# Performance work log

Hardware: AMD Instinct MI355X
Metric: run time of the kernel (lower is better)

## Reference

```python
import jax, jax.numpy as jnp
import numpy as np

B, I, H, O, K = 256, 512, 512, 512, 256


def setup_inputs() -> dict:
    key = jax.random.key(0)
    ks = jax.random.split(key, 16)
    def lin(kw, kb, out_dim, in_dim):
        s = 1.0 / np.sqrt(in_dim)
        W = jax.random.uniform(kw, (out_dim, in_dim), jnp.float32, -s, s)
        b = jax.random.uniform(kb, (out_dim,), jnp.float32, -s, s)
        return W, b
    Wd, bd = lin(ks[0], ks[1], H, I + 2 * H)
    Wr, br = lin(ks[2], ks[3], H, I + H)
    Wz, bz = lin(ks[4], ks[5], H, I + H)
    Wh, bh = lin(ks[6], ks[7], H, I + H)
    Wo, bo = lin(ks[8], ks[9], O, H)
    return {
        "sample": jax.random.normal(ks[10], (B, I), jnp.float32),
        "hidden": jax.random.normal(ks[11], (B, H), jnp.float32),
        "hidden_tensor": jax.random.normal(ks[12], (K, B, H), jnp.float32),
        "d_0": jax.random.normal(ks[13], (B, H), jnp.float32),
        "Wd": Wd, "bd": bd, "Wr": Wr, "br": br,
        "Wz": Wz, "bz": bz, "Wh": Wh, "bh": bh, "Wo": Wo, "bo": bo,
    }


def _filter_d(hidden_tensor, d_values):
    # get_ws: w[j] = prod_{m=0}^{K-1-j} (m - d) / (m + 1)  for j in [0, K)
    # Vectorized: cumprod of (m-d)/(m+1) along m, then flip.
    m = jnp.arange(K, dtype=d_values.dtype).reshape(K, 1, 1)  # [K,1,1]
    factors = (m - d_values[None, :, :]) / (m + 1.0)          # [K,B,H]
    w = jnp.flip(jnp.cumprod(factors, axis=0), axis=0)        # [K,B,H]
    return jnp.sum(hidden_tensor * w, axis=0)                 # [B,H]


def reference(sample, hidden, hidden_tensor, d_0,
              Wd, bd, Wr, br, Wz, bz, Wh, bh, Wo, bo):
    combined = jnp.concatenate([sample, hidden], axis=1)          # [B, I+H]
    combined_d = jnp.concatenate([sample, hidden, d_0], axis=1)   # [B, I+2H]

    d_values = jax.nn.sigmoid(combined_d @ Wd.T + bd) * 0.5       # [B,H]
    first = -_filter_d(hidden_tensor, d_values)                   # [B,H]

    r_gate = jax.nn.sigmoid(combined @ Wr.T + br)
    z_gate = jax.nn.sigmoid(combined @ Wz.T + bz)

    combined2 = jnp.concatenate([sample, r_gate * hidden], axis=1)
    h_tilde = jnp.tanh(combined2 @ Wh.T + bh)
    second = h_tilde * (1.0 - z_gate)

    hidden_new = first + second                                   # [B,H]
    h_c_1 = jnp.concatenate([hidden_tensor, hidden_new[None]], axis=0)[1:]  # [K,B,H]
    output = hidden_new @ Wo.T + bo                               # [B,O]
    return (output, hidden_new, h_c_1, d_values)
```

## Files before the change

### kernel.cpp

```cpp
#include <hip/hip_runtime.h>
#include <cstddef>

#define B_ 256
#define H_ 512
#define KF 256
#define BH 131072
#define BH2 65536
#define BH4 32768
#define H4 128

#define BM 64
#define BN 64
#define BK 16

__device__ __forceinline__ float sigmoidf_(float x) { return 1.0f / (1.0f + __expf(-x)); }
__device__ __forceinline__ float tanh_fast(float x) { return 2.0f / (1.0f + __expf(-2.0f * x)) - 1.0f; }
__device__ __forceinline__ float4 sig4(float4 v) {
    return make_float4(sigmoidf_(v.x), sigmoidf_(v.y), sigmoidf_(v.z), sigmoidf_(v.w));
}

#define MAC_LOOP()                                                         \
    _Pragma("unroll")                                                      \
    for (int kk = 0; kk < BK; ++kk) {                                      \
        const float4 a = *(const float4*)&As[kk][ty << 2];                 \
        const float4 w = *(const float4*)&Ws[kk][tx << 2];                 \
        const float a4[4] = {a.x, a.y, a.z, a.w};                          \
        const float w4[4] = {w.x, w.y, w.z, w.w};                          \
        _Pragma("unroll")                                                  \
        for (int i = 0; i < 4; ++i)                                        \
            _Pragma("unroll")                                              \
            for (int j = 0; j < 4; ++j)                                    \
                acc[i][j] = fmaf(a4[i], w4[j], acc[i][j]);                 \
    }

template<bool MUL>
__device__ __forceinline__ void gemm64(
    float (*As)[BM + 4], float (*Ws)[BN + 4],
    const float* __restrict__ abase, const float* __restrict__ rbase,
    const float* __restrict__ W, int Ktot, int ks,
    int bm, int bn, int nIter, float* __restrict__ p)
{
    const int tid = threadIdx.x;
    const int ty = tid >> 4, tx = tid & 15;
    const int lrow = tid >> 2, lcol = (tid & 3) << 2;
    const float* aptr = abase + (bm + lrow) * 512 + lcol;
    const float* rptr = MUL ? rbase + (bm + lrow) * 512 + lcol : nullptr;
    const float* wptr = W + (size_t)(bn + lrow) * Ktot + ks + lcol;

    float acc[4][4] = {};
    float4 av = *(const float4*)aptr;
    if (MUL) { const float4 rv = *(const float4*)rptr;
               av.x *= rv.x; av.y *= rv.y; av.z *= rv.z; av.w *= rv.w; }
    float4 wv = *(const float4*)wptr;

    for (int it = 0; it < nIter; ++it) {
        __syncthreads();
        As[lcol + 0][lrow] = av.x; As[lcol + 1][lrow] = av.y;
        As[lcol + 2][lrow] = av.z; As[lcol + 3][lrow] = av.w;
        Ws[lcol + 0][lrow] = wv.x; Ws[lcol + 1][lrow] = wv.y;
        Ws[lcol + 2][lrow] = wv.z; Ws[lcol + 3][lrow] = wv.w;
        __syncthreads();
        if (it < nIter - 1) {
            av = *(const float4*)(aptr + (it + 1) * BK);
            if (MUL) { const float4 rv = *(const float4*)(rptr + (it + 1) * BK);
                       av.x *= rv.x; av.y *= rv.y; av.z *= rv.z; av.w *= rv.w; }
            wv = *(const float4*)(wptr + (it + 1) * BK);
        }
        MAC_LOOP();
    }
    #pragma unroll
    for (int i = 0; i < 4; ++i) {
        const int m = bm + (ty << 2) + i;
        #pragma unroll
        for (int j = 0; j < 4; ++j)
            p[m * 512 + bn + (tx << 2) + j] = acc[i][j];
    }
}

__global__ __launch_bounds__(256) void k_gemm_drz(
    const float* __restrict__ sample, const float* __restrict__ hidden,
    const float* __restrict__ d0,
    const float* __restrict__ Wd, const float* __restrict__ Wr,
    const float* __restrict__ Wz,
    float* __restrict__ dbase, float* __restrict__ rzbase)
{
    __shared__ float As[BK][BM + 4];
    __shared__ float Ws[BK][BN + 4];
    const int z = blockIdx.z;
    if (z < 6) {
        const int ks = z << 8, seg = ks >> 9;
        const float* ab = (seg == 0 ? sample : (seg == 1 ? hidden : d0)) + (ks & 511);
        gemm64<false>(As, Ws, ab, nullptr, Wd, 1536, ks,
                      blockIdx.y * BM, blockIdx.x * BN, 16, dbase + (size_t)z * BH);
    } else {
        const int id = z - 6, gz = id >> 2, s = id & 3, ks = s << 8;
        const float* ab = (ks < 512 ? sample + ks : hidden + (ks - 512));
        gemm64<false>(As, Ws, ab, nullptr, gz ? Wz : Wr, 1024, ks,
                      blockIdx.y * BM, blockIdx.x * BN, 16, rzbase + (size_t)id * BH);
    }
}

__global__ __launch_bounds__(256) void k_dv(
    const float4* __restrict__ dparts, const float4* __restrict__ bd,
    const float4* __restrict__ rzparts, const float4* __restrict__ br,
    const float4* __restrict__ bz,
    float4* __restrict__ dv4, float4* __restrict__ rb4, float4* __restrict__ zb4)
{
    const int g = blockIdx.x * 256 + threadIdx.x;
    const int n = g & (H4 - 1);
    float4 sd = bd[n], sr = br[n], sz = bz[n];
    #pragma unroll
    for (int s = 0; s < 6; ++s) { const float4 p = dparts[(size_t)s * BH4 + g];
        sd.x += p.x; sd.y += p.y; sd.z += p.z; sd.w += p.w; }
    #pragma unroll
    for (int s = 0; s < 4; ++s) { const float4 p = rzparts[(size_t)s * BH4 + g];
        sr.x += p.x; sr.y += p.y; sr.z += p.z; sr.w += p.w; }
    #pragma unroll
    for (int s = 4; s < 8; ++s) { const float4 p = rzparts[(size_t)s * BH4 + g];
        sz.x += p.x; sz.y += p.y; sz.z += p.z; sz.w += p.w; }
    const float4 d = sig4(sd);
    dv4[g] = make_float4(0.5f * d.x, 0.5f * d.y, 0.5f * d.z, 0.5f * d.w);
    rb4[g] = sig4(sr);
    zb4[g] = sig4(sz);
}

__global__ __launch_bounds__(256) void k_gemm_h(
    const float* __restrict__ sample, const float* __restrict__ hidden,
    const float* __restrict__ rb, const float* __restrict__ Wh,
    float* __restrict__ parts)
{
    __shared__ float As[BK][BM + 4];
    __shared__ float Ws[BK][BN + 4];
    const int s = blockIdx.z, ks = s << 8;
    if (ks < 512)
        gemm64<false>(As, Ws, sample + ks, nullptr, Wh, 1024, ks,
                      blockIdx.y * BM, blockIdx.x * BN, 16, parts + (size_t)s * BH);
    else
        gemm64<true>(As, Ws, hidden + (ks - 512), rb + (ks - 512), Wh, 1024, ks,
                     blockIdx.y * BM, blockIdx.x * BN, 16, parts + (size_t)s * BH);
}

#define FLOADB(buf, b)                                                     \
    _Pragma("unroll")                                                      \
    for (int u = 0; u < 8; ++u)                                            \
        buf[u] = ld_base[-(ptrdiff_t)((b) * 8 + u) * BH4];

#define FCSTORE(buf, b)                                                    \
    _Pragma("unroll")                                                      \
    for (int u = 0; u < 8; ++u) {                                          \
        const int t = t0 + (b) * 8 + u;                                    \
        const float iv = s_inv[t], tv = s_tinv[t];                         \
        c.x *= fmaf(-d.x, iv, tv); c.y *= fmaf(-d.y, iv, tv);              \
        c.z *= fmaf(-d.z, iv, tv); c.w *= fmaf(-d.w, iv, tv);              \
        a.x = fmaf(buf[u].x, c.x, a.x); a.y = fmaf(buf[u].y, c.y, a.y);    \
        a.z = fmaf(buf[u].z, c.z, a.z); a.w = fmaf(buf[u].w, c.w, a.w);    \
        st_base[-(ptrdiff_t)((b) * 8 + u) * BH4] = buf[u];                 \
    }

__global__ __launch_bounds__(256) void k_filter(
    const float4* __restrict__ ht4, const float4* __restrict__ dv4,
    float4* __restrict__ acc_out, float4* __restrict__ hc14)
{
    __shared__ float s_inv[KF], s_tinv[KF];
    const int tid = threadIdx.x;
    const float fi = 1.0f / (float)(tid + 1);
    s_inv[tid] = fi; s_tinv[tid] = (float)tid * fi;
    __syncthreads();

    const int seg = blockIdx.x >> 7;
    const int q   = ((blockIdx.x & 127) << 8) | tid;
    const float4 d = dv4[q];
    const int t0 = seg << 6;

    const float4* ld_base = ht4 + (size_t)(255 - t0) * BH4 + q;
    float4*       st_base = hc14 + (ptrdiff_t)(254 - t0) * BH4 + q;

    float4 c = make_float4(1.f, 1.f, 1.f, 1.f);
    float4 a = make_float4(0.f, 0.f, 0.f, 0.f);

    float4 va[8], vb[8];
    FLOADB(va, 0);
    #pragma unroll
    for (int b = 0; b < 8; b += 2) {
        FLOADB(vb, b + 1);
        FCSTORE(va, b);
        if (b + 2 < 8) { FLOADB(va, b + 2); }
        FCSTORE(vb, b + 1);
    }
    acc_out[(size_t)seg * BH4 + q] = a;
}

__global__ __launch_bounds__(256) void k_finalize(
    const float4* __restrict__ dv4, const float4* __restrict__ ws4,
    const float4* __restrict__ bh, const float4* __restrict__ zb4,
    float4* hc1_4, float4* __restrict__ hn_out)
{
    __shared__ float s_inv[192], s_tinv[192];
    const int tid = threadIdx.x;
    if (tid < 192) { const float fi = 1.0f / (float)(tid + 1);
                     s_inv[tid] = fi; s_tinv[tid] = (float)tid * fi; }
    __syncthreads();

    const int g = blockIdx.x * 256 + tid;
    const int n = g & (H4 - 1);
    const float4 d = dv4[g];

    float4 c = make_float4(1.f, 1.f, 1.f, 1.f), px0, px1, px2;
    #pragma unroll 16
    for (int t = 0; t < 64; ++t) {
        const float iv = s_inv[t], tv = s_tinv[t];
        c.x *= fmaf(-d.x, iv, tv); c.y *= fmaf(-d.y, iv, tv);
        c.z *= fmaf(-d.z, iv, tv); c.w *= fmaf(-d.w, iv, tv);
    }
    px0 = c;
    #pragma unroll 16
    for (int t = 64; t < 128; ++t) {
        const float iv = s_inv[t], tv = s_tinv[t];
        c.x *= fmaf(-d.x, iv, tv); c.y *= fmaf(-d.y, iv, tv);
        c.z *= fmaf(-d.z, iv, tv); c.w *= fmaf(-d.w, iv, tv);
    }
    px1 = c;
    #pragma unroll 16
    for (int t = 128; t < 192; ++t) {
        const float iv = s_inv[t], tv = s_tinv[t];
        c.x *= fmaf(-d.x, iv, tv); c.y *= fmaf(-d.y, iv, tv);
        c.z *= fmaf(-d.z, iv, tv); c.w *= fmaf(-d.w, iv, tv);
    }
    px2 = c;

    const float4 a0 = ws4[(size_t)4 * BH4 + g];
    const float4 a1 = ws4[(size_t)5 * BH4 + g];
    const float4 a2 = ws4[(size_t)6 * BH4 + g];
    const float4 a3 = ws4[(size_t)7 * BH4 + g];
    float4 hs = bh[n];
    #pragma unroll
    for (int s = 0; s < 4; ++s) { const float4 p = ws4[(size_t)s * BH4 + g];
        hs.x += p.x; hs.y += p.y; hs.z += p.z; hs.w += p.w; }
    const float4 z = zb4[g];

    float4 hn;
    hn.x = tanh_fast(hs.x) * (1.0f - z.x)
         - (a0.x + px0.x * a1.x + px1.x * a2.x + px2.x * a3.x);
    hn.y = tanh_fast(hs.y) * (1.0f - z.y)
         - (a0.y + px0.y * a1.y + px1.y * a2.y + px2.y * a3.y);
    hn.z = tanh_fast(hs.z) * (1.0f - z.z)
         - (a0.z + px0.z * a1.z + px1.z * a2.z + px2.z * a3.z);
    hn.w = tanh_fast(hs.w) * (1.0f - z.w)
         - (a0.w + px0.w * a1.w + px1.w * a2.w + px2.w * a3.w);
    hn_out[g] = hn;
    hc1_4[(size_t)255 * BH4 + g] = hn;
}

__global__ __launch_bounds__(256) void k_gemm_o(
    const float* __restrict__ hn, const float* __restrict__ Wo,
    float* __restrict__ parts, int chunk)
{
    __shared__ float As[BK][BM + 4];
    __shared__ float Ws[BK][BN + 4];
    const int s = blockIdx.z, ks = s * chunk;
    gemm64<false>(As, Ws, hn + ks, nullptr, Wo, 512, ks,
                  blockIdx.y * BM, blockIdx.x * BN, chunk / BK, parts + (size_t)s * BH);
}

__global__ __launch_bounds__(256) void k_reduce_o(
    const float4* parts, const float4* __restrict__ bo, float4* out, int NS)
{
    const int g = blockIdx.x * 256 + threadIdx.x;
    float4 v = bo[g & (H4 - 1)];
    for (int s = 0; s < NS; ++s) { const float4 p = parts[(size_t)s * BH4 + g];
        v.x += p.x; v.y += p.y; v.z += p.z; v.w += p.w; }
    out[g] = v;
}

__global__ __launch_bounds__(256) void k_reduce_rz(
    const float4* __restrict__ parts, const float4* __restrict__ br,
    const float4* __restrict__ bz, float4* __restrict__ rb, float4* __restrict__ zb)
{
    const int g = blockIdx.x * 256 + threadIdx.x;
    const int n = g & (H4 - 1);
    float4 r = br[n], z = bz[n];
    #pragma unroll
    for (int s = 0; s < 4; ++s) { const float4 p = parts[(size_t)s * BH4 + g];
        r.x += p.x; r.y += p.y; r.z += p.z; r.w += p.w; }
    #pragma unroll
    for (int s = 4; s < 8; ++s) { const float4 p = parts[(size_t)s * BH4 + g];
        z.x += p.x; z.y += p.y; z.z += p.z; z.w += p.w; }
    rb[g] = sig4(r); zb[g] = sig4(z);
}

__global__ __launch_bounds__(256) void k_filter_full(
    const float* __restrict__ ht, const float* dparts, const float* __restrict__ bd,
    const float* zbuf, const float* hparts, const float* __restrict__ bh,
    float* hc1, float* __restrict__ dv_out, float* __restrict__ hn_out)
{
    __shared__ float s_inv[KF], s_tinv[KF];
    const int tid = threadIdx.x;
    const float fi = 1.0f / (float)(tid + 1);
    s_inv[tid] = fi; s_tinv[tid] = (float)tid * fi;
    __syncthreads();

    const int g = blockIdx.x * 256 + tid;
    const int n = g & (H_ - 1);
    float sd = bd[n];
    #pragma unroll
    for (int s = 0; s < 6; ++s) sd += dparts[(size_t)s * BH + g];
    const float d = 0.5f * sigmoidf_(sd);
    dv_out[g] = d;
    float sh = bh[n];
    #pragma unroll
    for (int s = 0; s < 4; ++s) sh += hparts[(size_t)s * BH + g];
    const float z = zbuf[g];

    float c = 1.0f, acc = 0.0f;
    #pragma unroll 16
    for (int t = 0; t < KF; ++t) {
        const int k = KF - 1 - t;
        const float v = ht[(size_t)k * BH + g];
        c *= fmaf(-d, s_inv[t], s_tinv[t]);
        acc = fmaf(v, c, acc);
        if (k >= 1) hc1[(size_t)(k - 1) * BH + g] = v;
    }
    const float hn = tanh_fast(sh) * (1.0f - z) - acc;
    hc1[(size_t)(KF - 1) * BH + g] = hn;
    hn_out[g] = hn;
}

extern "C" void kernel_launch(void* const* d_in, const int* in_sizes, int n_in,
                              void* d_out, int out_size, void* d_ws, size_t ws_size,
                              hipStream_t stream)
{
    const float* sample = (const float*)d_in[0];
    const float* hidden = (const float*)d_in[1];
    const float* ht     = (const float*)d_in[2];
    const float* d0     = (const float*)d_in[3];
    const float* Wd = (const float*)d_in[4];
    const float* bd = (const float*)d_in[5];
    const float* Wr = (const float*)d_in[6];
    const float* br = (const float*)d_in[7];
    const float* Wz = (const float*)d_in[8];
    const float* bz = (const float*)d_in[9];
    const float* Wh = (const float*)d_in[10];
    const float* bh = (const float*)d_in[11];
    const float* Wo = (const float*)d_in[12];
    const float* bo = (const float*)d_in[13];

    float* out     = (float*)d_out;
    float* out_o   = out;
    float* out_hn  = out + BH;
    float* out_hc1 = out + 2 * BH;
    float* out_dv  = out + 2 * BH + (size_t)KF * BH;

    const size_t slice = BH;
    const size_t need = 10ull * slice * sizeof(float);

    if (ws_size >= need) {
        float* ws = (float*)d_ws;
        float* rb = ws + 8 * slice;
        float* zb = ws + 9 * slice;

        k_gemm_drz<<<dim3(8, 4, 14), 256, 0, stream>>>(sample, hidden, d0,
                                                       Wd, Wr, Wz, out_hc1, ws);
        k_dv<<<dim3(128), 256, 0, stream>>>(
            (const float4*)out_hc1, (const float4*)bd,
            (const float4*)ws, (const float4*)br, (const float4*)bz,
            (float4*)out_dv, (float4*)rb, (float4*)zb);
        k_gemm_h<<<dim3(8, 4, 4), 256, 0, stream>>>(sample, hidden, rb, Wh, ws);
        k_filter<<<dim3(512), 256, 0, stream>>>(
            (const float4*)ht, (const float4*)out_dv,
            (float4*)(ws + 4 * slice), (float4*)out_hc1);
        k_finalize<<<dim3(128), 256, 0, stream>>>(
            (const float4*)out_dv, (const float4*)ws,
            (const float4*)bh, (const float4*)zb,
            (float4*)out_hc1, (float4*)out_hn);
        k_gemm_o<<<dim3(8, 4, 4), 256, 0, stream>>>(out_hn, Wo, ws, 128);
        k_reduce_o<<<dim3(128), 256, 0, stream>>>((const float4*)ws,
                                                  (const float4*)bo,
                                                  (float4*)out_o, 4);
    } else {
        float* sl = out_hc1;
        k_gemm_drz<<<dim3(8, 4, 14), 256, 0, stream>>>(sample, hidden, d0,
                                                       Wd, Wr, Wz, sl, sl + 6 * slice);
        k_reduce_rz<<<dim3(128), 256, 0, stream>>>((const float4*)(sl + 6 * slice),
                                                   (const float4*)br, (const float4*)bz,
                                                   (float4*)(sl + 14 * slice),
                                                   (float4*)(sl + 15 * slice));
        k_gemm_h<<<dim3(8, 4, 4), 256, 0, stream>>>(sample, hidden, sl + 14 * slice, Wh,
                                                    sl + 16 * slice);
        k_filter_full<<<dim3(512), 256, 0, stream>>>(ht, sl, bd, sl + 15 * slice,
                                                     sl + 16 * slice, bh,
                                                     out_hc1, out_dv, out_hn);
        k_gemm_o<<<dim3(8, 4, 1), 256, 0, stream>>>(out_hn, Wo, out_o, 512);
        k_reduce_o<<<dim3(128), 256, 0, stream>>>((const float4*)out_o, (const float4*)bo,
                                                  (float4*)out_o, 1);
    }
}
```

Measured before the change: 101.8 us.

## Merge h-gate GEMM and filter into one launch with finer filter segments

Combines the Wh GEMM and the fractional filter pass into one kernel. The first 128 blocks run the GEMM and the rest run the filter, so the compute-bound GEMM overlaps the bandwidth-bound copy and reduction of hidden_tensor. The filter is split into 8 segments of 32 steps instead of 4 of 64, which gives more parallelism, and it writes h_c_1 with nontemporal stores. The finalize kernel now chains 7 segment prefix products, and the workspace requirement grows from 10 to 14 slices, which could push execution onto the fallback path if the workspace is small.

```diff
diff --git a/kernel.cpp b/kernel.cpp
--- a/kernel.cpp
+++ b/kernel.cpp
@@ -12,6 +12,8 @@
 #define BM 64
 #define BN 64
 #define BK 16
+
+typedef float nf4 __attribute__((ext_vector_type(4)));
 
 __device__ __forceinline__ float sigmoidf_(float x) { return 1.0f / (1.0f + __expf(-x)); }
 __device__ __forceinline__ float tanh_fast(float x) { return 2.0f / (1.0f + __expf(-2.0f * x)) - 1.0f; }
@@ -124,6 +126,159 @@
     zb4[g] = sig4(sz);
 }
 
+#define FLOADB(buf, b)                                                     \
+    _Pragma("unroll")                                                      \
+    for (int u = 0; u < 8; ++u)                                            \
+        buf[u] = ld_base[-(ptrdiff_t)((b) * 8 + u) * BH4];
+
+#define FCSTORE(buf, b)                                                    \
+    _Pragma("unroll")                                                      \
+    for (int u = 0; u < 8; ++u) {                                          \
+        const int t = t0 + (b) * 8 + u;                                    \
+        const float iv = s_inv[t], tv = s_tinv[t];                         \
+        c.x *= fmaf(-d.x, iv, tv); c.y *= fmaf(-d.y, iv, tv);              \
+        c.z *= fmaf(-d.z, iv, tv); c.w *= fmaf(-d.w, iv, tv);              \
+        a.x = fmaf(buf[u].x, c.x, a.x); a.y = fmaf(buf[u].y, c.y, a.y);    \
+        a.z = fmaf(buf[u].z, c.z, a.z); a.w = fmaf(buf[u].w, c.w, a.w);    \
+        __builtin_nontemporal_store(*(const nf4*)&buf[u],                  \
+            (nf4*)(st_base - (ptrdiff_t)((b) * 8 + u) * BH4));             \
+    }
+
+__global__ __launch_bounds__(256, 4) void k_mega(
+    const float4* __restrict__ ht4, const float4* __restrict__ dv4,
+    const float* __restrict__ sample, const float* __restrict__ hidden,
+    const float* __restrict__ rb, const float* __restrict__ Wh,
+    float* __restrict__ ws, float4* __restrict__ hc14)
+{
+    if (blockIdx.x < 128) {
+        __shared__ float As[BK][BM + 4];
+        __shared__ float Wsh[BK][BN + 4];
+        const int id = blockIdx.x;
+        const int s = id >> 5, t2 = id & 31;
+        const int bn = (t2 >> 2) << 6, bm = (t2 & 3) << 6, ks = s << 8;
+        if (ks < 512)
+            gemm64<false>(As, Wsh, sample + ks, nullptr, Wh, 1024, ks, bm, bn, 16,
+                          ws + (size_t)s * BH);
+        else
+            gemm64<true>(As, Wsh, hidden + (ks - 512), rb + (ks - 512), Wh, 1024, ks,
+                         bm, bn, 16, ws + (size_t)s * BH);
+        return;
+    }
+    __shared__ float s_inv[KF], s_tinv[KF];
+    const int tid = threadIdx.x;
+    const float fi = 1.0f / (float)(tid + 1);
+    s_inv[tid] = fi; s_tinv[tid] = (float)tid * fi;
+    __syncthreads();
+
+    const int fb  = blockIdx.x - 128;
+    const int seg = fb >> 7;
+    const int q   = ((fb & 127) << 8) | tid;
+    const float4 d = dv4[q];
+    const int t0 = seg << 5;
+
+    const float4* ld_base = ht4 + (size_t)(255 - t0) * BH4 + q;
+    float4*       st_base = hc14 + (ptrdiff_t)(254 - t0) * BH4 + q;
+
+    float4 c = make_float4(1.f, 1.f, 1.f, 1.f);
+    float4 a = make_float4(0.f, 0.f, 0.f, 0.f);
+
+    float4 va[8], vb[8];
+    FLOADB(va, 0);
+    FLOADB(vb, 1);
+    FCSTORE(va, 0);
+    FLOADB(va, 2);
+    FCSTORE(vb, 1);
+    FLOADB(vb, 3);
+    FCSTORE(va, 2);
+    FCSTORE(vb, 3);
+
+    const int slice = (seg < 4) ? (4 + seg) : (6 + seg);
+    ((float4*)ws)[(size_t)slice * BH4 + q] = a;
+}
+
+__global__ __launch_bounds__(256) void k_finalize(
+    const float4* __restrict__ dv4, const float4* __restrict__ ws4,
+    const float4* __restrict__ bh, const float4* __restrict__ zb4,
+    float4* hc1_4, float4* __restrict__ hn_out)
+{
+    __shared__ float s_inv[224], s_tinv[224];
+    const int tid = threadIdx.x;
+    if (tid < 224) { const float fi = 1.0f / (float)(tid + 1);
+                     s_inv[tid] = fi; s_tinv[tid] = (float)tid * fi; }
+    __syncthreads();
+
+    const int g = blockIdx.x * 256 + tid;
+    const int n = g & (H4 - 1);
+    const float4 d = dv4[g];
+
+    float4 acc = ws4[(size_t)4 * BH4 + g];
+    float4 c = make_float4(1.f, 1.f, 1.f, 1.f);
+    #pragma unroll
+    for (int sgm = 1; sgm < 8; ++sgm) {
+        #pragma unroll
+        for (int t = (sgm - 1) * 32; t < sgm * 32; ++t) {
+            const float iv = s_inv[t], tv = s_tinv[t];
+            c.x *= fmaf(-d.x, iv, tv); c.y *= fmaf(-d.y, iv, tv);
+            c.z *= fmaf(-d.z, iv, tv); c.w *= fmaf(-d.w, iv, tv);
+        }
+        const int sl = (sgm < 4) ? (4 + sgm) : (6 + sgm);
+        const float4 ai = ws4[(size_t)sl * BH4 + g];
+        acc.x = fmaf(c.x, ai.x, acc.x); acc.y = fmaf(c.y, ai.y, acc.y);
+        acc.z = fmaf(c.z, ai.z, acc.z); acc.w = fmaf(c.w, ai.w, acc.w);
+    }
+
+    float4 hs = bh[n];
+    #pragma unroll
+    for (int s = 0; s < 4; ++s) { const float4 p = ws4[(size_t)s * BH4 + g];
+        hs.x += p.x; hs.y += p.y; hs.z += p.z; hs.w += p.w; }
+    const float4 z = zb4[g];
+
+    float4 hn;
+    hn.x = tanh_fast(hs.x) * (1.0f - z.x) - acc.x;
+    hn.y = tanh_fast(hs.y) * (1.0f - z.y) - acc.y;
+    hn.z = tanh_fast(hs.z) * (1.0f - z.z) - acc.z;
+    hn.w = tanh_fast(hs.w) * (1.0f - z.w) - acc.w;
+    hn_out[g] = hn;
+    hc1_4[(size_t)255 * BH4 + g] = hn;
+}
+
+__global__ __launch_bounds__(256) void k_gemm_o(
+    const float* __restrict__ hn, const float* __restrict__ Wo,
+    float* __restrict__ parts, int chunk)
+{
+    __shared__ float As[BK][BM + 4];
+    __shared__ float Ws[BK][BN + 4];
+    const int s = blockIdx.z, ks = s * chunk;
+    gemm64<false>(As, Ws, hn + ks, nullptr, Wo, 512, ks,
+                  blockIdx.y * BM, blockIdx.x * BN, chunk / BK, parts + (size_t)s * BH);
+}
+
+__global__ __launch_bounds__(256) void k_reduce_o(
+    const float4* parts, const float4* __restrict__ bo, float4* out, int NS)
+{
+    const int g = blockIdx.x * 256 + threadIdx.x;
+    float4 v = bo[g & (H4 - 1)];
+    for (int s = 0; s < NS; ++s) { const float4 p = parts[(size_t)s * BH4 + g];
+        v.x += p.x; v.y += p.y; v.z += p.z; v.w += p.w; }
+    out[g] = v;
+}
+
+__global__ __launch_bounds__(256) void k_reduce_rz(
+    const float4* __restrict__ parts, const float4* __restrict__ br,
+    const float4* __restrict__ bz, float4* __restrict__ rb, float4* __restrict__ zb)
+{
+    const int g = blockIdx.x * 256 + threadIdx.x;
+    const int n = g & (H4 - 1);
+    float4 r = br[n], z = bz[n];
+    #pragma unroll
+    for (int s = 0; s < 4; ++s) { const float4 p = parts[(size_t)s * BH4 + g];
+        r.x += p.x; r.y += p.y; r.z += p.z; r.w += p.w; }
+    #pragma unroll
+    for (int s = 4; s < 8; ++s) { const float4 p = parts[(size_t)s * BH4 + g];
+        z.x += p.x; z.y += p.y; z.z += p.z; z.w += p.w; }
+    rb[g] = sig4(r); zb[g] = sig4(z);
+}
+
 __global__ __launch_bounds__(256) void k_gemm_h(
     const float* __restrict__ sample, const float* __restrict__ hidden,
     const float* __restrict__ rb, const float* __restrict__ Wh,
@@ -138,154 +293,6 @@
     else
         gemm64<true>(As, Ws, hidden + (ks - 512), rb + (ks - 512), Wh, 1024, ks,
                      blockIdx.y * BM, blockIdx.x * BN, 16, parts + (size_t)s * BH);
-}
-
-#define FLOADB(buf, b)                                                     \
-    _Pragma("unroll")                                                      \
-    for (int u = 0; u < 8; ++u)                                            \
-        buf[u] = ld_base[-(ptrdiff_t)((b) * 8 + u) * BH4];
-
-#define FCSTORE(buf, b)                                                    \
-    _Pragma("unroll")                                                      \
-    for (int u = 0; u < 8; ++u) {                                          \
-        const int t = t0 + (b) * 8 + u;                                    \
-        const float iv = s_inv[t], tv = s_tinv[t];                         \
-        c.x *= fmaf(-d.x, iv, tv); c.y *= fmaf(-d.y, iv, tv);              \
-        c.z *= fmaf(-d.z, iv, tv); c.w *= fmaf(-d.w, iv, tv);              \
-        a.x = fmaf(buf[u].x, c.x, a.x); a.y = fmaf(buf[u].y, c.y, a.y);    \
-        a.z = fmaf(buf[u].z, c.z, a.z); a.w = fmaf(buf[u].w, c.w, a.w);    \
-        st_base[-(ptrdiff_t)((b) * 8 + u) * BH4] = buf[u];                 \
-    }
-
-__global__ __launch_bounds__(256) void k_filter(
-    const float4* __restrict__ ht4, const float4* __restrict__ dv4,
-    float4* __restrict__ acc_out, float4* __restrict__ hc14)
-{
-    __shared__ float s_inv[KF], s_tinv[KF];
-    const int tid = threadIdx.x;
-    const float fi = 1.0f / (float)(tid + 1);
-    s_inv[tid] = fi; s_tinv[tid] = (float)tid * fi;
-    __syncthreads();
-
-    const int seg = blockIdx.x >> 7;
-    const int q   = ((blockIdx.x & 127) << 8) | tid;
-    const float4 d = dv4[q];
-    const int t0 = seg << 6;
-
-    const float4* ld_base = ht4 + (size_t)(255 - t0) * BH4 + q;
-    float4*       st_base = hc14 + (ptrdiff_t)(254 - t0) * BH4 + q;
-
-    float4 c = make_float4(1.f, 1.f, 1.f, 1.f);
-    float4 a = make_float4(0.f, 0.f, 0.f, 0.f);
-
-    float4 va[8], vb[8];
-    FLOADB(va, 0);
-    #pragma unroll
-    for (int b = 0; b < 8; b += 2) {
-        FLOADB(vb, b + 1);
-        FCSTORE(va, b);
-        if (b + 2 < 8) { FLOADB(va, b + 2); }
-        FCSTORE(vb, b + 1);
-    }
-    acc_out[(size_t)seg * BH4 + q] = a;
-}
-
-__global__ __launch_bounds__(256) void k_finalize(
-    const float4* __restrict__ dv4, const float4* __restrict__ ws4,
-    const float4* __restrict__ bh, const float4* __restrict__ zb4,
-    float4* hc1_4, float4* __restrict__ hn_out)
-{
-    __shared__ float s_inv[192], s_tinv[192];
-    const int tid = threadIdx.x;
-    if (tid < 192) { const float fi = 1.0f / (float)(tid + 1);
-                     s_inv[tid] = fi; s_tinv[tid] = (float)tid * fi; }
-    __syncthreads();
-
-    const int g = blockIdx.x * 256 + tid;
-    const int n = g & (H4 - 1);
-    const float4 d = dv4[g];
-
-    float4 c = make_float4(1.f, 1.f, 1.f, 1.f), px0, px1, px2;
-    #pragma unroll 16
-    for (int t = 0; t < 64; ++t) {
-        const float iv = s_inv[t], tv = s_tinv[t];
-        c.x *= fmaf(-d.x, iv, tv); c.y *= fmaf(-d.y, iv, tv);
-        c.z *= fmaf(-d.z, iv, tv); c.w *= fmaf(-d.w, iv, tv);
-    }
-    px0 = c;
-    #pragma unroll 16
-    for (int t = 64; t < 128; ++t) {
-        const float iv = s_inv[t], tv = s_tinv[t];
-        c.x *= fmaf(-d.x, iv, tv); c.y *= fmaf(-d.y, iv, tv);
-        c.z *= fmaf(-d.z, iv, tv); c.w *= fmaf(-d.w, iv, tv);
-    }
-    px1 = c;
-    #pragma unroll 16
-    for (int t = 128; t < 192; ++t) {
-        const float iv = s_inv[t], tv = s_tinv[t];
-        c.x *= fmaf(-d.x, iv, tv); c.y *= fmaf(-d.y, iv, tv);
-        c.z *= fmaf(-d.z, iv, tv); c.w *= fmaf(-d.w, iv, tv);
-    }
-    px2 = c;
-
-    const float4 a0 = ws4[(size_t)4 * BH4 + g];
-    const float4 a1 = ws4[(size_t)5 * BH4 + g];
-    const float4 a2 = ws4[(size_t)6 * BH4 + g];
-    const float4 a3 = ws4[(size_t)7 * BH4 + g];
-    float4 hs = bh[n];
-    #pragma unroll
-    for (int s = 0; s < 4; ++s) { const float4 p = ws4[(size_t)s * BH4 + g];
-        hs.x += p.x; hs.y += p.y; hs.z += p.z; hs.w += p.w; }
-    const float4 z = zb4[g];
-
-    float4 hn;
-    hn.x = tanh_fast(hs.x) * (1.0f - z.x)
-         - (a0.x + px0.x * a1.x + px1.x * a2.x + px2.x * a3.x);
-    hn.y = tanh_fast(hs.y) * (1.0f - z.y)
-         - (a0.y + px0.y * a1.y + px1.y * a2.y + px2.y * a3.y);
-    hn.z = tanh_fast(hs.z) * (1.0f - z.z)
-         - (a0.z + px0.z * a1.z + px1.z * a2.z + px2.z * a3.z);
-    hn.w = tanh_fast(hs.w) * (1.0f - z.w)
-         - (a0.w + px0.w * a1.w + px1.w * a2.w + px2.w * a3.w);
-    hn_out[g] = hn;
-    hc1_4[(size_t)255 * BH4 + g] = hn;
-}
-
-__global__ __launch_bounds__(256) void k_gemm_o(
-    const float* __restrict__ hn, const float* __restrict__ Wo,
-    float* __restrict__ parts, int chunk)
-{
-    __shared__ float As[BK][BM + 4];
-    __shared__ float Ws[BK][BN + 4];
-    const int s = blockIdx.z, ks = s * chunk;
-    gemm64<false>(As, Ws, hn + ks, nullptr, Wo, 512, ks,
-                  blockIdx.y * BM, blockIdx.x * BN, chunk / BK, parts + (size_t)s * BH);
-}
-
-__global__ __launch_bounds__(256) void k_reduce_o(
-    const float4* parts, const float4* __restrict__ bo, float4* out, int NS)
-{
-    const int g = blockIdx.x * 256 + threadIdx.x;
-    float4 v = bo[g & (H4 - 1)];
-    for (int s = 0; s < NS; ++s) { const float4 p = parts[(size_t)s * BH4 + g];
-        v.x += p.x; v.y += p.y; v.z += p.z; v.w += p.w; }
-    out[g] = v;
-}
-
-__global__ __launch_bounds__(256) void k_reduce_rz(
-    const float4* __restrict__ parts, const float4* __restrict__ br,
-    const float4* __restrict__ bz, float4* __restrict__ rb, float4* __restrict__ zb)
-{
-    const int g = blockIdx.x * 256 + threadIdx.x;
-    const int n = g & (H4 - 1);
-    float4 r = br[n], z = bz[n];
-    #pragma unroll
-    for (int s = 0; s < 4; ++s) { const float4 p = parts[(size_t)s * BH4 + g];
-        r.x += p.x; r.y += p.y; r.z += p.z; r.w += p.w; }
-    #pragma unroll
-    for (int s = 4; s < 8; ++s) { const float4 p = parts[(size_t)s * BH4 + g];
-        z.x += p.x; z.y += p.y; z.z += p.z; z.w += p.w; }
-    rb[g] = sig4(r); zb[g] = sig4(z);
 }
 
 __global__ __launch_bounds__(256) void k_filter_full(
@@ -351,7 +358,7 @@
     float* out_dv  = out + 2 * BH + (size_t)KF * BH;
 
     const size_t slice = BH;
-    const size_t need = 10ull * slice * sizeof(float);
+    const size_t need = 14ull * slice * sizeof(float);
 
     if (ws_size >= need) {
         float* ws = (float*)d_ws;
@@ -364,10 +371,9 @@
             (const float4*)out_hc1, (const float4*)bd,
             (const float4*)ws, (const float4*)br, (const float4*)bz,
             (float4*)out_dv, (float4*)rb, (float4*)zb);
-        k_gemm_h<<<dim3(8, 4, 4), 256, 0, stream>>>(sample, hidden, rb, Wh, ws);
-        k_filter<<<dim3(512), 256, 0, stream>>>(
-            (const float4*)ht, (const float4*)out_dv,
-            (float4*)(ws + 4 * slice), (float4*)out_hc1);
+        k_mega<<<dim3(1152), 256, 0, stream>>>(
+            (const float4*)ht, (const float4*)out_dv, sample, hidden, rb, Wh,
+            ws, (float4*)out_hc1);
         k_finalize<<<dim3(128), 256, 0, stream>>>(
             (const float4*)out_dv, (const float4*)ws,
             (const float4*)bh, (const float4*)zb,
```

Result: faster. 84.96 us (-16.6%).
